# Kernel optimization log

Measured on AMD Instinct MI355X. Metric: run time of the kernel, lower is better.

The kernel has to match this reference:

```python
import jax, jax.numpy as jnp
import numpy as np
from jax import lax

HID, STATE, K, EXPAND = 1024, 16, 4, 2
INNER = EXPAND * HID
B_SZ, L = 4, 4096


def setup_inputs() -> dict:
    key = jax.random.key(0)
    ks = jax.random.split(key, 16)
    s = 0.02
    return {
        "x": jax.random.normal(ks[0], (B_SZ, L, HID), dtype=jnp.float32),
        "in_proj_w": jax.random.normal(ks[1], (2 * INNER, HID), dtype=jnp.float32) * s,
        "in_proj_b": jnp.zeros((2 * INNER,), jnp.float32),
        "conv_w": jax.random.normal(ks[2], (INNER, 1, K), dtype=jnp.float32) * s,
        "conv_b": jnp.zeros((INNER,), jnp.float32),
        "dt_w": jax.random.normal(ks[3], (INNER, INNER), dtype=jnp.float32) * s,
        "dt_b": jnp.zeros((INNER,), jnp.float32),
        "A_log": jnp.log(jnp.abs(jax.random.normal(ks[4], (INNER, STATE), dtype=jnp.float32)) + 1e-6),
        "B_w": jax.random.normal(ks[5], (STATE, INNER), dtype=jnp.float32) * s,
        "B_b": jnp.zeros((STATE,), jnp.float32),
        "C_w": jax.random.normal(ks[6], (STATE, INNER), dtype=jnp.float32) * s,
        "C_b": jnp.zeros((STATE,), jnp.float32),
        "D": jnp.ones((INNER,), jnp.float32),
        "out_w": jax.random.normal(ks[7], (HID, INNER), dtype=jnp.float32) * s,
        "out_b": jnp.zeros((HID,), jnp.float32),
    }


def _selective_scan(x, dt, A, Bm, Cm, D):
    # x, dt: (B, L, inner); A: (inner, state); Bm, Cm: (B, L, state); D: (inner,)
    def step(h, inp):
        x_t, dt_t, B_t, C_t = inp  # (B,inner),(B,inner),(B,state),(B,state)
        dA = jnp.exp(dt_t[:, :, None] * A[None, :, :])          # (B, inner, state)
        dB = dt_t[:, :, None] * B_t[:, None, :]                  # (B, inner, state)
        h = dA * h + dB * x_t[:, :, None]
        y = jnp.einsum("bds,bs->bd", h, C_t) + D * x_t
        return h, y

    B_, _, d = x.shape
    h0 = jnp.zeros((B_, d, A.shape[1]), x.dtype)
    xs = (jnp.swapaxes(x, 0, 1), jnp.swapaxes(dt, 0, 1),
          jnp.swapaxes(Bm, 0, 1), jnp.swapaxes(Cm, 0, 1))
    _, ys = lax.scan(step, h0, xs)  # ys: (L, B, inner)
    return jnp.swapaxes(ys, 0, 1)


def reference(x, in_proj_w, in_proj_b, conv_w, conv_b, dt_w, dt_b,
              A_log, B_w, B_b, C_w, C_b, D, out_w, out_b):
    xz = x @ in_proj_w.T + in_proj_b                 # (B, L, 2*inner)
    x_part, z = jnp.split(xz, 2, axis=-1)
    # causal depthwise conv1d: torch pads both sides K-1 then truncates to L -> left pad only
    xc = lax.conv_general_dilated(
        jnp.swapaxes(x_part, 1, 2), conv_w,
        window_strides=(1,), padding=[(K - 1, 0)],
        dimension_numbers=("NCH", "OIH", "NCH"),
        feature_group_count=INNER) + conv_b[None, :, None]
    x_conv = jax.nn.silu(jnp.swapaxes(xc, 1, 2))     # (B, L, inner)
    A = -jnp.exp(A_log)
    dt = jax.nn.softplus(x_conv @ dt_w.T + dt_b)
    Bm = x_conv @ B_w.T + B_b                        # (B, L, state)
    Cm = x_conv @ C_w.T + C_b
    y = _selective_scan(x_conv, dt, A, Bm, Cm, D)
    y = y * jax.nn.silu(z)
    return y @ out_w.T + out_b
```

## Files before the change

kernel.cpp:

```cpp
#include <hip/hip_runtime.h>
#include <hip/hip_bf16.h>

#define HID   1024
#define STATE 16
#define KCONV 4
#define INNER 2048
#define BSZ   4
#define LSEQ  4096
#define BL    (BSZ * LSEQ)
#define NCAT  2304
#define NCH   64
#define TC    64

typedef unsigned short ushort_t;
typedef unsigned int   uint_t;
typedef __attribute__((ext_vector_type(8))) __bf16 bf16x8;
typedef __attribute__((ext_vector_type(4))) float  f32x4;
typedef __attribute__((ext_vector_type(8))) unsigned short u16x8;

__device__ __forceinline__ ushort_t f2bf(float f) {
    uint_t u = __float_as_uint(f);
    u += 0x7fffu + ((u >> 16) & 1u);
    return (ushort_t)(u >> 16);
}
__device__ __forceinline__ float bf2f(ushort_t h) {
    return __uint_as_float(((uint_t)h) << 16);
}

#define AS1 __attribute__((address_space(1)))
#define AS3 __attribute__((address_space(3)))
__device__ __forceinline__ void async_copy16(const ushort_t* g, ushort_t* l) {
    __builtin_amdgcn_global_load_lds((const AS1 void*)g, (AS3 void*)l, 16, 0, 0);
}

__global__ void cast_bf16_kernel(const float* __restrict__ src, ushort_t* __restrict__ dst, int n) {
    int i = blockIdx.x * 256 + threadIdx.x;
    if (i < n) dst[i] = f2bf(src[i]);
}

__global__ void build_wcat_kernel(const float* __restrict__ dtw, const float* __restrict__ Bw,
                                  const float* __restrict__ Cw, ushort_t* __restrict__ out) {
    int i = blockIdx.x * 256 + threadIdx.x;
    if (i >= NCAT * INNER) return;
    int r = i >> 11;
    int k = i & (INNER - 1);
    float v = 0.f;
    if (r < INNER)            v = dtw[i];
    else if (r < INNER + 16)  v = Bw[(r - INNER) * INNER + k];
    else if (r < INNER + 32)  v = Cw[(r - INNER - 16) * INNER + k];
    out[i] = f2bf(v);
}

__global__ void build_biascat_kernel(const float* __restrict__ dtb, const float* __restrict__ Bb,
                                     const float* __restrict__ Cb, float* __restrict__ out) {
    int i = blockIdx.x * 256 + threadIdx.x;
    if (i >= NCAT) return;
    float v = 0.f;
    if (i < INNER)            v = dtb[i];
    else if (i < INNER + 16)  v = Bb[i - INNER];
    else if (i < INNER + 32)  v = Cb[i - INNER - 16];
    out[i] = v;
}

#define mfma_bf16 __builtin_amdgcn_mfma_f32_16x16x32_bf16

template <int MODE, int KK>
__global__ __launch_bounds__(512, 2) void gemm256_kernel(
    const ushort_t* __restrict__ A, const ushort_t* __restrict__ Bw,
    const float* __restrict__ bias,
    ushort_t* __restrict__ oU0, ushort_t* __restrict__ oU1,
    float* __restrict__ oF, float* __restrict__ oB, float* __restrict__ oC,
    int N)
{
    __shared__ ushort_t smem[65536];

    const int tid  = threadIdx.x;
    const int w    = tid >> 6;
    const int lane = tid & 63;
    const int m16  = lane & 15;
    const int ko   = lane >> 4;
    const int wm   = w >> 2;
    const int wn   = w & 3;
    const int wnh  = wn >> 1;

    const int gx   = gridDim.x;
    const int lb   = blockIdx.y * gx + blockIdx.x;
    const int xcd  = lb & 7;
    const int slot = lb >> 3;
    const int tx   = slot % gx;
    const int ty   = xcd * 8 + slot / gx;
    const int row0 = ty * 256;
    const int col0 = tx * 256;

    constexpr int NKT = KK >> 6;

    const size_t Lofs = (size_t)(w * 16 + (lane >> 3)) * KK
                      + (size_t)(((lane & 7) ^ (lane >> 3)) << 3);
    const ushort_t* pA = A  + (size_t)row0 * KK + Lofs;
    const ushort_t* pB = Bw + (size_t)col0 * KK + Lofs;

    f32x4 acc[8][4] = {};

    auto stage_half = [&](int j, int tau) {
        const int sb = ((tau & 1) << 15) | (j << 13);
        const ushort_t* px = (j < 2) ? pB : pA;
#pragma unroll
        for (int i = 0; i < 2; i++) {
            const ushort_t* s = px + (size_t)((j & 1) * 128 + i * 8) * KK + (tau << 6);
            async_copy16(s, &smem[sb + w * 1024 + i * 512]);
        }
    };
    auto ldA = [&](int buf, int rf, int s) -> bf16x8 {
        const int row = (rf << 4) + m16;
        const int c16 = ((s << 2) + ko) ^ (row & 7);
        return *(const bf16x8*)&smem[(buf << 15) + ((2 + wm) << 13) + (row << 6) + (c16 << 3)];
    };
    auto ldB = [&](int buf, int cf, int s) -> bf16x8 {
        const int row = ((wn & 1) << 6) + (cf << 4) + m16;
        const int c16 = ((s << 2) + ko) ^ (row & 7);
        return *(const bf16x8*)&smem[(buf << 15) + (wnh << 13) + (row << 6) + (c16 << 3)];
    };

    stage_half(0, 0); stage_half(1, 0); stage_half(2, 0); stage_half(3, 0);
    stage_half(0, 1); stage_half(1, 1);
    asm volatile("s_waitcnt vmcnt(4)" ::: "memory");
    __builtin_amdgcn_s_barrier();

#pragma unroll 1
    for (int t = 0; t < NKT; ++t) {
        const int buf = t & 1;
        bf16x8 aF[4][2], bC0[2][2], bC1[2][2];

#pragma unroll
        for (int r = 0; r < 4; r++) { aF[r][0] = ldA(buf, r, 0); aF[r][1] = ldA(buf, r, 1); }
#pragma unroll
        for (int c = 0; c < 2; c++) { bC0[c][0] = ldB(buf, c, 0); bC0[c][1] = ldB(buf, c, 1); }
        if (t + 1 < NKT) stage_half(2, t + 1);
        __builtin_amdgcn_s_barrier();
        __builtin_amdgcn_s_setprio(1);
#pragma unroll
        for (int r = 0; r < 4; r++)
#pragma unroll
            for (int c = 0; c < 2; c++) {
                acc[r][c] = mfma_bf16(aF[r][0], bC0[c][0], acc[r][c], 0, 0, 0);
                acc[r][c] = mfma_bf16(aF[r][1], bC0[c][1], acc[r][c], 0, 0, 0);
            }
        __builtin_amdgcn_s_setprio(0);
        __builtin_amdgcn_s_barrier();

#pragma unroll
        for (int c = 0; c < 2; c++) { bC1[c][0] = ldB(buf, 2 + c, 0); bC1[c][1] = ldB(buf, 2 + c, 1); }
        if (t + 1 < NKT) stage_half(3, t + 1);
        __builtin_amdgcn_s_barrier();
        __builtin_amdgcn_s_setprio(1);
#pragma unroll
        for (int r = 0; r < 4; r++)
#pragma unroll
            for (int c = 0; c < 2; c++) {
                acc[r][2 + c] = mfma_bf16(aF[r][0], bC1[c][0], acc[r][2 + c], 0, 0, 0);
                acc[r][2 + c] = mfma_bf16(aF[r][1], bC1[c][1], acc[r][2 + c], 0, 0, 0);
            }
        __builtin_amdgcn_s_setprio(0);
        __builtin_amdgcn_s_barrier();

#pragma unroll
        for (int r = 0; r < 4; r++) { aF[r][0] = ldA(buf, 4 + r, 0); aF[r][1] = ldA(buf, 4 + r, 1); }
        if (t + 2 < NKT) stage_half(0, t + 2);
        __builtin_amdgcn_s_barrier();
        __builtin_amdgcn_s_setprio(1);
#pragma unroll
        for (int r = 0; r < 4; r++)
#pragma unroll
            for (int c = 0; c < 2; c++) {
                acc[4 + r][2 + c] = mfma_bf16(aF[r][0], bC1[c][0], acc[4 + r][2 + c], 0, 0, 0);
                acc[4 + r][2 + c] = mfma_bf16(aF[r][1], bC1[c][1], acc[4 + r][2 + c], 0, 0, 0);
            }
        __builtin_amdgcn_s_setprio(0);
        __builtin_amdgcn_s_barrier();

        if (t + 2 < NKT) stage_half(1, t + 2);
        __builtin_amdgcn_s_barrier();
        __builtin_amdgcn_s_setprio(1);
#pragma unroll
        for (int r = 0; r < 4; r++)
#pragma unroll
            for (int c = 0; c < 2; c++) {
                acc[4 + r][c] = mfma_bf16(aF[r][0], bC0[c][0], acc[4 + r][c], 0, 0, 0);
                acc[4 + r][c] = mfma_bf16(aF[r][1], bC0[c][1], acc[4 + r][c], 0, 0, 0);
            }
        __builtin_amdgcn_s_setprio(0);
        if (t + 1 < NKT) {
            if (t + 1 == NKT - 1) asm volatile("s_waitcnt vmcnt(0)" ::: "memory");
            else                  asm volatile("s_waitcnt vmcnt(4)" ::: "memory");
            __builtin_amdgcn_s_barrier();
        }
    }

    const int rbase = (lane >> 4) * 4;
    __syncthreads();

    if (MODE == 2) {
#pragma unroll
        for (int i = 0; i < 8; i++)
#pragma unroll
            for (int j = 0; j < 4; j++)
#pragma unroll
                for (int r = 0; r < 4; r++) {
                    int row = row0 + wm * 128 + i * 16 + rbase + r;
                    int col = col0 + wn * 64 + j * 16 + m16;
                    oF[(size_t)row * N + col] = acc[i][j][r] + bias[col];
                }
    } else if (MODE == 1 && col0 >= INNER) {
#pragma unroll
        for (int i = 0; i < 8; i++)
#pragma unroll
            for (int j = 0; j < 4; j++)
#pragma unroll
                for (int r = 0; r < 4; r++) {
                    int row = row0 + wm * 128 + i * 16 + rbase + r;
                    int col = col0 + wn * 64 + j * 16 + m16;
                    float v = acc[i][j][r] + bias[col];
                    if (col < INNER + 16)      oB[(size_t)row * STATE + (col - INNER)] = v;
                    else if (col < INNER + 32) oC[(size_t)row * STATE + (col - INNER - 16)] = v;
                }
    } else {
        const bool isZ = (MODE == 0) && (col0 >= INNER);
        ushort_t* my = &smem[w * 8192];
        const int SW = 68;
#pragma unroll
        for (int p = 0; p < 2; p++) {
#pragma unroll
            for (int i4 = 0; i4 < 4; i4++)
#pragma unroll
                for (int j = 0; j < 4; j++)
#pragma unroll
                    for (int r = 0; r < 4; r++) {
                        int lr = i4 * 16 + rbase + r;
                        int lc = j * 16 + m16;
                        float v = acc[p * 4 + i4][j][r] + bias[col0 + wn * 64 + lc];
                        ushort_t o;
                        if (MODE == 0) {
                            if (isZ) { float s = v / (1.f + __expf(-v)); o = f2bf(s); }
                            else     { o = f2bf(v); }
                        } else {
                            float sp = fmaxf(v, 0.f) + log1pf(__expf(-fabsf(v)));
                            o = f2bf(sp);
                        }
                        my[lr * SW + lc] = o;
                    }
            __builtin_amdgcn_sched_barrier(0);
#pragma unroll
            for (int it = 0; it < 8; it++) {
                int lr = it * 8 + (lane >> 3);
                u16x8 vv = *(const u16x8*)&my[lr * SW + (lane & 7) * 8];
                int grow = row0 + wm * 128 + p * 64 + lr;
                int gcol = col0 + wn * 64 + (lane & 7) * 8;
                if (MODE == 0 && isZ)
                    *(u16x8*)&oU1[(size_t)grow * INNER + (gcol - INNER)] = vv;
                else
                    *(u16x8*)&oU0[(size_t)grow * INNER + gcol] = vv;
            }
            __builtin_amdgcn_sched_barrier(0);
        }
    }
}

__global__ void conv_silu_kernel(const ushort_t* __restrict__ xp, const float* __restrict__ cw,
                                 const float* __restrict__ cb,
                                 ushort_t* __restrict__ xcbf) {
    int i = blockIdx.x * 256 + threadIdx.x;
    int base = i * 8;
    int d0 = base & (INNER - 1);
    int bl = base >> 11;
    int l  = bl & (LSEQ - 1);

    f32x4 wv[8];
    float acc[8];
#pragma unroll
    for (int j = 0; j < 8; j++) {
        wv[j]  = *(const f32x4*)&cw[(d0 + j) * KCONV];
        acc[j] = cb[d0 + j];
    }
#pragma unroll
    for (int k = 0; k < KCONV; k++) {
        int ls = l - (KCONV - 1) + k;
        if (ls >= 0) {
            u16x8 v = *(const u16x8*)&xp[base + (ls - l) * INNER];
#pragma unroll
            for (int j = 0; j < 8; j++) acc[j] = fmaf(wv[j][k], bf2f(v[j]), acc[j]);
        }
    }
    u16x8 o;
#pragma unroll
    for (int j = 0; j < 8; j++) {
        float s = acc[j] / (1.f + __expf(-acc[j]));
        o[j] = f2bf(s);
    }
    *(u16x8*)&xcbf[base] = o;
}

__global__ __launch_bounds__(256) void scan_pass1(
    const ushort_t* __restrict__ dt, const ushort_t* __restrict__ xc,
    const float* __restrict__ Bm, const float* __restrict__ A_log,
    ushort_t* __restrict__ Pc, float* __restrict__ Sc)
{
    const int b = blockIdx.z;
    const int c = blockIdx.y;
    const int d = blockIdx.x * 256 + threadIdx.x;

    float A[STATE], h[STATE];
    {
        float al[STATE];
#pragma unroll
        for (int q = 0; q < 4; q++)
            *(f32x4*)(al + q * 4) = *(const f32x4*)(A_log + (size_t)d * STATE + q * 4);
#pragma unroll
        for (int s = 0; s < STATE; s++) { A[s] = -__expf(al[s]); h[s] = 0.f; }
    }
    float sdt = 0.f;
    const size_t base = (size_t)b * LSEQ + (size_t)c * TC;

#pragma unroll 2
    for (int t = 0; t < TC; t++) {
        const size_t r = base + t;
        const float dtv = bf2f(dt[r * INNER + d]);
        const float xv  = bf2f(xc[r * INNER + d]);
        const float dtx = dtv * xv;
        float Bv[STATE];
#pragma unroll
        for (int q = 0; q < 4; q++)
            *(f32x4*)(Bv + q * 4) = *(const f32x4*)(Bm + r * STATE + q * 4);
        sdt += dtv;
#pragma unroll
        for (int s = 0; s < STATE; s++) {
            const float dA = __expf(dtv * A[s]);
            h[s] = fmaf(dA, h[s], dtx * Bv[s]);
        }
    }

    const size_t idx = ((size_t)(b * NCH + c) * INNER + d) * STATE;
#pragma unroll
    for (int q = 0; q < 4; q++)
        *(f32x4*)(Sc + idx + q * 4) = *(const f32x4*)(h + q * 4);
    u16x8 p0, p1;
#pragma unroll
    for (int s = 0; s < 8; s++) { p0[s] = f2bf(__expf(A[s] * sdt)); }
#pragma unroll
    for (int s = 0; s < 8; s++) { p1[s] = f2bf(__expf(A[s + 8] * sdt)); }
    *(u16x8*)(Pc + idx)     = p0;
    *(u16x8*)(Pc + idx + 8) = p1;
}

__global__ __launch_bounds__(256) void scan_pass2(
    const ushort_t* __restrict__ Pc, float* Sc)
{
    const int i = blockIdx.x * 256 + threadIdx.x;
    const int b   = i >> 15;
    const int rem = i & (INNER * STATE - 1);
    float H = 0.f;
#pragma unroll 8
    for (int c = 0; c < NCH; c++) {
        const size_t idx = (size_t)(b * NCH + c) * (INNER * STATE) + rem;
        const float Pv = bf2f(Pc[idx]);
        const float Sv = Sc[idx];
        const float Hn = fmaf(Pv, H, Sv);
        Sc[idx] = H;
        H = Hn;
    }
}

__global__ __launch_bounds__(256) void scan_pass3(
    const ushort_t* __restrict__ dt, const ushort_t* __restrict__ xc,
    const float* __restrict__ Bm, const float* __restrict__ Cm,
    const float* __restrict__ A_log, const float* __restrict__ Dv,
    const float* __restrict__ Hc, ushort_t* sz_y)
{
    const int b = blockIdx.z;
    const int c = blockIdx.y;
    const int d = blockIdx.x * 256 + threadIdx.x;

    float A[STATE], h[STATE];
    {
        float al[STATE];
#pragma unroll
        for (int q = 0; q < 4; q++)
            *(f32x4*)(al + q * 4) = *(const f32x4*)(A_log + (size_t)d * STATE + q * 4);
#pragma unroll
        for (int s = 0; s < STATE; s++) A[s] = -__expf(al[s]);
    }
    const size_t hidx = ((size_t)(b * NCH + c) * INNER + d) * STATE;
#pragma unroll
    for (int q = 0; q < 4; q++)
        *(f32x4*)(h + q * 4) = *(const f32x4*)(Hc + hidx + q * 4);

    const float Dd = Dv[d];
    const size_t base = (size_t)b * LSEQ + (size_t)c * TC;

#pragma unroll 2
    for (int t = 0; t < TC; t++) {
        const size_t r = base + t;
        const float dtv = bf2f(dt[r * INNER + d]);
        const float xv  = bf2f(xc[r * INNER + d]);
        const float dtx = dtv * xv;
        float Bv[STATE], Cv[STATE];
#pragma unroll
        for (int q = 0; q < 4; q++) {
            *(f32x4*)(Bv + q * 4) = *(const f32x4*)(Bm + r * STATE + q * 4);
            *(f32x4*)(Cv + q * 4) = *(const f32x4*)(Cm + r * STATE + q * 4);
        }
        float y = Dd * xv;
#pragma unroll
        for (int s = 0; s < STATE; s++) {
            const float dA = __expf(dtv * A[s]);
            h[s] = fmaf(dA, h[s], dtx * Bv[s]);
            y = fmaf(h[s], Cv[s], y);
        }
        const float zv = bf2f(sz_y[r * INNER + d]);
        sz_y[r * INNER + d] = f2bf(y * zv);
    }
}

extern "C" void kernel_launch(void* const* d_in, const int* in_sizes, int n_in,
                              void* d_out, int out_size, void* d_ws, size_t ws_size,
                              hipStream_t stream) {
    const float* x       = (const float*)d_in[0];
    const float* in_w    = (const float*)d_in[1];
    const float* in_b    = (const float*)d_in[2];
    const float* conv_w  = (const float*)d_in[3];
    const float* conv_b  = (const float*)d_in[4];
    const float* dt_w    = (const float*)d_in[5];
    const float* dt_b    = (const float*)d_in[6];
    const float* A_log   = (const float*)d_in[7];
    const float* B_w     = (const float*)d_in[8];
    const float* B_b     = (const float*)d_in[9];
    const float* C_w     = (const float*)d_in[10];
    const float* C_b     = (const float*)d_in[11];
    const float* Dv      = (const float*)d_in[12];
    const float* out_w   = (const float*)d_in[13];
    const float* out_b   = (const float*)d_in[14];
    float* out = (float*)d_out;

    char* ws = (char*)d_ws;
    size_t off = 0;
    auto alloc = [&](size_t bytes) { size_t o = off; off += (bytes + 255) & ~(size_t)255; return o; };

    ushort_t* Xbf     = (ushort_t*)(ws + alloc((size_t)BL * HID * 2));
    ushort_t* W1bf    = (ushort_t*)(ws + alloc((size_t)2 * INNER * HID * 2));
    ushort_t* Wcat    = (ushort_t*)(ws + alloc((size_t)NCAT * INNER * 2));
    ushort_t* Woutbf  = (ushort_t*)(ws + alloc((size_t)HID * INNER * 2));
    float*    biascat = (float*)   (ws + alloc((size_t)NCAT * 4));
    ushort_t* xpart   = (ushort_t*)(ws + alloc((size_t)BL * INNER * 2));
    ushort_t* szbf    = (ushort_t*)(ws + alloc((size_t)BL * INNER * 2));
    ushort_t* xconvbf = (ushort_t*)(ws + alloc((size_t)BL * INNER * 2));
    float*    Bmbuf   = (float*)   (ws + alloc((size_t)BL * STATE * 4));
    float*    Cmbuf   = (float*)   (ws + alloc((size_t)BL * STATE * 4));
    ushort_t* dtbuf   = xpart;

    ushort_t* Pbuf = (ushort_t*)ws;
    float*    Sbuf = (float*)(ws + (size_t)NCH * BSZ * INNER * STATE * 2);
    (void)in_sizes; (void)n_in; (void)out_size;

    if (ws_size < off) return;

    {
        int n = BL * HID;
        cast_bf16_kernel<<<(n + 255) / 256, 256, 0, stream>>>(x, Xbf, n);
        n = 2 * INNER * HID;
        cast_bf16_kernel<<<(n + 255) / 256, 256, 0, stream>>>(in_w, W1bf, n);
        n = HID * INNER;
        cast_bf16_kernel<<<(n + 255) / 256, 256, 0, stream>>>(out_w, Woutbf, n);
        n = NCAT * INNER;
        build_wcat_kernel<<<(n + 255) / 256, 256, 0, stream>>>(dt_w, B_w, C_w, Wcat);
        build_biascat_kernel<<<(NCAT + 255) / 256, 256, 0, stream>>>(dt_b, B_b, C_b, biascat);
    }

    gemm256_kernel<0, HID><<<dim3((2 * INNER) / 256, BL / 256), 512, 0, stream>>>(
        Xbf, W1bf, in_b, xpart, szbf, nullptr, nullptr, nullptr, 2 * INNER);

    conv_silu_kernel<<<(BL * INNER / 8) / 256, 256, 0, stream>>>(xpart, conv_w, conv_b, xconvbf);

    gemm256_kernel<1, INNER><<<dim3(NCAT / 256, BL / 256), 512, 0, stream>>>(
        xconvbf, Wcat, biascat, dtbuf, nullptr, nullptr, Bmbuf, Cmbuf, NCAT);

    scan_pass1<<<dim3(INNER / 256, NCH, BSZ), 256, 0, stream>>>(
        dtbuf, xconvbf, Bmbuf, A_log, Pbuf, Sbuf);
    scan_pass2<<<(BSZ * INNER * STATE) / 256, 256, 0, stream>>>(Pbuf, Sbuf);
    scan_pass3<<<dim3(INNER / 256, NCH, BSZ), 256, 0, stream>>>(
        dtbuf, xconvbf, Bmbuf, Cmbuf, A_log, Dv, Sbuf, szbf);

    gemm256_kernel<2, INNER><<<dim3(HID / 256, BL / 256), 512, 0, stream>>>(
        szbf, Woutbf, out_b, nullptr, nullptr, out, nullptr, nullptr, HID);
}
```

Baseline: 1.032 ms.

## Shrink GEMM tiles to 256x128 with simpler double-buffered K loop

The GEMM tile width drops from 256 to 128 columns, so twice as many blocks launch and LDS use per block falls. The wavefront-quadrant pipeline with staggered half-stage prefetch and setprio is replaced by a plain double buffer: the whole next K tile is fetched each iteration, followed by a full vmcnt(0) wait. The concatenated dt/B/C weight is trimmed from 2304 to 2176 columns, cutting padded work in the second GEMM. The aim is better occupancy and less padding, at the cost of lower arithmetic intensity per tile and less overlap of loads with MFMA.

```diff
diff --git a/kernel.cpp b/kernel.cpp
--- a/kernel.cpp
+++ b/kernel.cpp
@@ -8,7 +8,7 @@
 #define BSZ   4
 #define LSEQ  4096
 #define BL    (BSZ * LSEQ)
-#define NCAT  2304
+#define NCAT  2176
 #define NCH   64
 #define TC    64
 
@@ -72,7 +72,7 @@
     float* __restrict__ oF, float* __restrict__ oB, float* __restrict__ oC,
     int N)
 {
-    __shared__ ushort_t smem[65536];
+    __shared__ ushort_t smem[49152];
 
     const int tid  = threadIdx.x;
     const int w    = tid >> 6;
@@ -81,7 +81,6 @@
     const int ko   = lane >> 4;
     const int wm   = w >> 2;
     const int wn   = w & 3;
-    const int wnh  = wn >> 1;
 
     const int gx   = gridDim.x;
     const int lb   = blockIdx.y * gx + blockIdx.x;
@@ -90,7 +89,7 @@
     const int tx   = slot % gx;
     const int ty   = xcd * 8 + slot / gx;
     const int row0 = ty * 256;
-    const int col0 = tx * 256;
+    const int col0 = tx * 128;
 
     constexpr int NKT = KK >> 6;
 
@@ -99,99 +98,54 @@
     const ushort_t* pA = A  + (size_t)row0 * KK + Lofs;
     const ushort_t* pB = Bw + (size_t)col0 * KK + Lofs;
 
-    f32x4 acc[8][4] = {};
-
-    auto stage_half = [&](int j, int tau) {
-        const int sb = ((tau & 1) << 15) | (j << 13);
-        const ushort_t* px = (j < 2) ? pB : pA;
-#pragma unroll
-        for (int i = 0; i < 2; i++) {
-            const ushort_t* s = px + (size_t)((j & 1) * 128 + i * 8) * KK + (tau << 6);
-            async_copy16(s, &smem[sb + w * 1024 + i * 512]);
+    f32x4 acc[8][2] = {};
+
+    auto stage_tile = [&](int tau) {
+        const int bb = (tau & 1) * 24576;
+        const int k0 = tau << 6;
+#pragma unroll
+        for (int j = 0; j < 3; j++) {
+            const ushort_t* px = (j == 0) ? pB : pA + (size_t)((j - 1) << 7) * KK;
+#pragma unroll
+            for (int i = 0; i < 2; i++) {
+                const ushort_t* s = px + (size_t)(i * 8) * KK + k0;
+                async_copy16(s, &smem[bb + j * 8192 + w * 1024 + i * 512]);
+            }
         }
     };
     auto ldA = [&](int buf, int rf, int s) -> bf16x8 {
         const int row = (rf << 4) + m16;
         const int c16 = ((s << 2) + ko) ^ (row & 7);
-        return *(const bf16x8*)&smem[(buf << 15) + ((2 + wm) << 13) + (row << 6) + (c16 << 3)];
+        return *(const bf16x8*)&smem[buf * 24576 + (1 + wm) * 8192 + (row << 6) + (c16 << 3)];
     };
     auto ldB = [&](int buf, int cf, int s) -> bf16x8 {
-        const int row = ((wn & 1) << 6) + (cf << 4) + m16;
+        const int row = (wn << 5) + (cf << 4) + m16;
         const int c16 = ((s << 2) + ko) ^ (row & 7);
-        return *(const bf16x8*)&smem[(buf << 15) + (wnh << 13) + (row << 6) + (c16 << 3)];
+        return *(const bf16x8*)&smem[buf * 24576 + (row << 6) + (c16 << 3)];
     };
 
-    stage_half(0, 0); stage_half(1, 0); stage_half(2, 0); stage_half(3, 0);
-    stage_half(0, 1); stage_half(1, 1);
-    asm volatile("s_waitcnt vmcnt(4)" ::: "memory");
+    stage_tile(0);
+    asm volatile("s_waitcnt vmcnt(0)" ::: "memory");
     __builtin_amdgcn_s_barrier();
 
 #pragma unroll 1
     for (int t = 0; t < NKT; ++t) {
         const int buf = t & 1;
-        bf16x8 aF[4][2], bC0[2][2], bC1[2][2];
-
-#pragma unroll
-        for (int r = 0; r < 4; r++) { aF[r][0] = ldA(buf, r, 0); aF[r][1] = ldA(buf, r, 1); }
-#pragma unroll
-        for (int c = 0; c < 2; c++) { bC0[c][0] = ldB(buf, c, 0); bC0[c][1] = ldB(buf, c, 1); }
-        if (t + 1 < NKT) stage_half(2, t + 1);
-        __builtin_amdgcn_s_barrier();
-        __builtin_amdgcn_s_setprio(1);
-#pragma unroll
-        for (int r = 0; r < 4; r++)
-#pragma unroll
-            for (int c = 0; c < 2; c++) {
-                acc[r][c] = mfma_bf16(aF[r][0], bC0[c][0], acc[r][c], 0, 0, 0);
-                acc[r][c] = mfma_bf16(aF[r][1], bC0[c][1], acc[r][c], 0, 0, 0);
+        if (t + 1 < NKT) stage_tile(t + 1);
+
+#pragma unroll
+        for (int s = 0; s < 2; s++) {
+            const bf16x8 b0 = ldB(buf, 0, s);
+            const bf16x8 b1 = ldB(buf, 1, s);
+#pragma unroll
+            for (int rf = 0; rf < 8; rf++) {
+                const bf16x8 a = ldA(buf, rf, s);
+                acc[rf][0] = mfma_bf16(a, b0, acc[rf][0], 0, 0, 0);
+                acc[rf][1] = mfma_bf16(a, b1, acc[rf][1], 0, 0, 0);
             }
-        __builtin_amdgcn_s_setprio(0);
-        __builtin_amdgcn_s_barrier();
-
-#pragma unroll
-        for (int c = 0; c < 2; c++) { bC1[c][0] = ldB(buf, 2 + c, 0); bC1[c][1] = ldB(buf, 2 + c, 1); }
-        if (t + 1 < NKT) stage_half(3, t + 1);
-        __builtin_amdgcn_s_barrier();
-        __builtin_amdgcn_s_setprio(1);
-#pragma unroll
-        for (int r = 0; r < 4; r++)
-#pragma unroll
-            for (int c = 0; c < 2; c++) {
-                acc[r][2 + c] = mfma_bf16(aF[r][0], bC1[c][0], acc[r][2 + c], 0, 0, 0);
-                acc[r][2 + c] = mfma_bf16(aF[r][1], bC1[c][1], acc[r][2 + c], 0, 0, 0);
-            }
-        __builtin_amdgcn_s_setprio(0);
-        __builtin_amdgcn_s_barrier();
-
-#pragma unroll
-        for (int r = 0; r < 4; r++) { aF[r][0] = ldA(buf, 4 + r, 0); aF[r][1] = ldA(buf, 4 + r, 1); }
-        if (t + 2 < NKT) stage_half(0, t + 2);
-        __builtin_amdgcn_s_barrier();
-        __builtin_amdgcn_s_setprio(1);
-#pragma unroll
-        for (int r = 0; r < 4; r++)
-#pragma unroll
-            for (int c = 0; c < 2; c++) {
-                acc[4 + r][2 + c] = mfma_bf16(aF[r][0], bC1[c][0], acc[4 + r][2 + c], 0, 0, 0);
-                acc[4 + r][2 + c] = mfma_bf16(aF[r][1], bC1[c][1], acc[4 + r][2 + c], 0, 0, 0);
-            }
-        __builtin_amdgcn_s_setprio(0);
-        __builtin_amdgcn_s_barrier();
-
-        if (t + 2 < NKT) stage_half(1, t + 2);
-        __builtin_amdgcn_s_barrier();
-        __builtin_amdgcn_s_setprio(1);
-#pragma unroll
-        for (int r = 0; r < 4; r++)
-#pragma unroll
-            for (int c = 0; c < 2; c++) {
-                acc[4 + r][c] = mfma_bf16(aF[r][0], bC0[c][0], acc[4 + r][c], 0, 0, 0);
-                acc[4 + r][c] = mfma_bf16(aF[r][1], bC0[c][1], acc[4 + r][c], 0, 0, 0);
-            }
-        __builtin_amdgcn_s_setprio(0);
+        }
         if (t + 1 < NKT) {
-            if (t + 1 == NKT - 1) asm volatile("s_waitcnt vmcnt(0)" ::: "memory");
-            else                  asm volatile("s_waitcnt vmcnt(4)" ::: "memory");
+            asm volatile("s_waitcnt vmcnt(0)" ::: "memory");
             __builtin_amdgcn_s_barrier();
         }
     }
@@ -201,66 +155,62 @@
 
     if (MODE == 2) {
 #pragma unroll
-        for (int i = 0; i < 8; i++)
-#pragma unroll
-            for (int j = 0; j < 4; j++)
+        for (int rf = 0; rf < 8; rf++)
+#pragma unroll
+            for (int cf = 0; cf < 2; cf++)
 #pragma unroll
                 for (int r = 0; r < 4; r++) {
-                    int row = row0 + wm * 128 + i * 16 + rbase + r;
-                    int col = col0 + wn * 64 + j * 16 + m16;
-                    oF[(size_t)row * N + col] = acc[i][j][r] + bias[col];
+                    int row = row0 + wm * 128 + rf * 16 + rbase + r;
+                    int col = col0 + wn * 32 + cf * 16 + m16;
+                    oF[(size_t)row * N + col] = acc[rf][cf][r] + bias[col];
                 }
     } else if (MODE == 1 && col0 >= INNER) {
 #pragma unroll
-        for (int i = 0; i < 8; i++)
-#pragma unroll
-            for (int j = 0; j < 4; j++)
+        for (int rf = 0; rf < 8; rf++)
+#pragma unroll
+            for (int cf = 0; cf < 2; cf++)
 #pragma unroll
                 for (int r = 0; r < 4; r++) {
-                    int row = row0 + wm * 128 + i * 16 + rbase + r;
-                    int col = col0 + wn * 64 + j * 16 + m16;
-                    float v = acc[i][j][r] + bias[col];
+                    int row = row0 + wm * 128 + rf * 16 + rbase + r;
+                    int col = col0 + wn * 32 + cf * 16 + m16;
+                    float v = acc[rf][cf][r] + bias[col];
                     if (col < INNER + 16)      oB[(size_t)row * STATE + (col - INNER)] = v;
                     else if (col < INNER + 32) oC[(size_t)row * STATE + (col - INNER - 16)] = v;
                 }
     } else {
         const bool isZ = (MODE == 0) && (col0 >= INNER);
-        ushort_t* my = &smem[w * 8192];
-        const int SW = 68;
-#pragma unroll
-        for (int p = 0; p < 2; p++) {
-#pragma unroll
-            for (int i4 = 0; i4 < 4; i4++)
-#pragma unroll
-                for (int j = 0; j < 4; j++)
-#pragma unroll
-                    for (int r = 0; r < 4; r++) {
-                        int lr = i4 * 16 + rbase + r;
-                        int lc = j * 16 + m16;
-                        float v = acc[p * 4 + i4][j][r] + bias[col0 + wn * 64 + lc];
-                        ushort_t o;
-                        if (MODE == 0) {
-                            if (isZ) { float s = v / (1.f + __expf(-v)); o = f2bf(s); }
-                            else     { o = f2bf(v); }
-                        } else {
-                            float sp = fmaxf(v, 0.f) + log1pf(__expf(-fabsf(v)));
-                            o = f2bf(sp);
-                        }
-                        my[lr * SW + lc] = o;
+        ushort_t* my = &smem[w * 4608];
+        const int SW = 36;
+#pragma unroll
+        for (int rf = 0; rf < 8; rf++)
+#pragma unroll
+            for (int cf = 0; cf < 2; cf++)
+#pragma unroll
+                for (int r = 0; r < 4; r++) {
+                    int lr = rf * 16 + rbase + r;
+                    int lc = cf * 16 + m16;
+                    float v = acc[rf][cf][r] + bias[col0 + wn * 32 + lc];
+                    ushort_t o;
+                    if (MODE == 0) {
+                        if (isZ) { float s = v / (1.f + __expf(-v)); o = f2bf(s); }
+                        else     { o = f2bf(v); }
+                    } else {
+                        float sp = fmaxf(v, 0.f) + log1pf(__expf(-fabsf(v)));
+                        o = f2bf(sp);
                     }
-            __builtin_amdgcn_sched_barrier(0);
-#pragma unroll
-            for (int it = 0; it < 8; it++) {
-                int lr = it * 8 + (lane >> 3);
-                u16x8 vv = *(const u16x8*)&my[lr * SW + (lane & 7) * 8];
-                int grow = row0 + wm * 128 + p * 64 + lr;
-                int gcol = col0 + wn * 64 + (lane & 7) * 8;
-                if (MODE == 0 && isZ)
-                    *(u16x8*)&oU1[(size_t)grow * INNER + (gcol - INNER)] = vv;
-                else
-                    *(u16x8*)&oU0[(size_t)grow * INNER + gcol] = vv;
-            }
-            __builtin_amdgcn_sched_barrier(0);
+                    my[lr * SW + lc] = o;
+                }
+        __builtin_amdgcn_sched_barrier(0);
+#pragma unroll
+        for (int it = 0; it < 8; it++) {
+            int lr = it * 16 + (lane >> 2);
+            u16x8 vv = *(const u16x8*)&my[lr * SW + (lane & 3) * 8];
+            int grow = row0 + wm * 128 + lr;
+            int gcol = col0 + wn * 32 + (lane & 3) * 8;
+            if (MODE == 0 && isZ)
+                *(u16x8*)&oU1[(size_t)grow * INNER + (gcol - INNER)] = vv;
+            else
+                *(u16x8*)&oU0[(size_t)grow * INNER + gcol] = vv;
         }
     }
 }
@@ -474,12 +424,12 @@
         build_biascat_kernel<<<(NCAT + 255) / 256, 256, 0, stream>>>(dt_b, B_b, C_b, biascat);
     }
 
-    gemm256_kernel<0, HID><<<dim3((2 * INNER) / 256, BL / 256), 512, 0, stream>>>(
+    gemm256_kernel<0, HID><<<dim3((2 * INNER) / 128, BL / 256), 512, 0, stream>>>(
         Xbf, W1bf, in_b, xpart, szbf, nullptr, nullptr, nullptr, 2 * INNER);
 
     conv_silu_kernel<<<(BL * INNER / 8) / 256, 256, 0, stream>>>(xpart, conv_w, conv_b, xconvbf);
 
-    gemm256_kernel<1, INNER><<<dim3(NCAT / 256, BL / 256), 512, 0, stream>>>(
+    gemm256_kernel<1, INNER><<<dim3(NCAT / 128, BL / 256), 512, 0, stream>>>(
         xconvbf, Wcat, biascat, dtbuf, nullptr, nullptr, Bmbuf, Cmbuf, NCAT);
 
     scan_pass1<<<dim3(INNER / 256, NCH, BSZ), 256, 0, stream>>>(
@@ -488,6 +438,6 @@
     scan_pass3<<<dim3(INNER / 256, NCH, BSZ), 256, 0, stream>>>(
         dtbuf, xconvbf, Bmbuf, Cmbuf, A_log, Dv, Sbuf, szbf);
 
-    gemm256_kernel<2, INNER><<<dim3(HID / 256, BL / 256), 512, 0, stream>>>(
+    gemm256_kernel<2, INNER><<<dim3(HID / 128, BL / 256), 512, 0, stream>>>(
         szbf, Woutbf, out_b, nullptr, nullptr, out, nullptr, nullptr, HID);
 }
```

Measured after the change: 1.055 ms. +2.2%, slower.
